# Kernel tuning notes

Hardware: AMD Instinct MI355X
Metric: run time of the kernel (lower is better)

The kernel has to match this reference:

```python
import jax, jax.numpy as jnp
import numpy as np


def _conv1x1(x, w, b):
    # x: (b, c_in, t, h, w); w: (c_out, c_in); b: (c_out,)
    return jnp.einsum('bcthw,oc->bothw', x, w) + b[None, :, None, None, None]


def _maxpool_hw(x):
    # MaxPool3d(kernel=(1,2,2)): pool spatial dims by 2 (h, w assumed even)
    b, c, t, h, w = x.shape
    return x.reshape(b, c, t, h // 2, 2, w // 2, 2).max(axis=(4, 6))


def setup_inputs() -> dict:
    key = jax.random.key(0)
    ks = jax.random.split(key, 9)
    C, CI = 256, 128  # in_channels, inter_channels = in_channels // 2
    B, T, H, W = 8, 8, 28, 28
    s = 1.0 / np.sqrt(C)
    si = 1.0 / np.sqrt(CI)
    return {
        'x': jax.random.normal(ks[0], (B, C, T, H, W), jnp.float32),
        'g_w': jax.random.normal(ks[1], (CI, C), jnp.float32) * s,
        'g_b': jax.random.normal(ks[2], (CI,), jnp.float32) * 0.01,
        'theta_w': jax.random.normal(ks[3], (CI, C), jnp.float32) * s,
        'theta_b': jax.random.normal(ks[4], (CI,), jnp.float32) * 0.01,
        'phi_w': jax.random.normal(ks[5], (CI, C), jnp.float32) * s,
        'phi_b': jax.random.normal(ks[6], (CI,), jnp.float32) * 0.01,
        'W_w': jax.random.normal(ks[7], (C, CI), jnp.float32) * si,
        'W_b': jax.random.normal(ks[8], (C,), jnp.float32) * 0.01,
    }


def reference(x, g_w, g_b, theta_w, theta_b, phi_w, phi_b, W_w, W_b):
    b, c, t, h, w = x.shape
    ci = g_w.shape[0]
    # g and phi paths are sub-sampled by MaxPool3d(1,2,2)
    g_x = _maxpool_hw(_conv1x1(x, g_w, g_b)).reshape(b, ci, -1)          # (b, ci, M)
    g_x = g_x.transpose(0, 2, 1)                                          # (b, M, ci)
    theta_x = _conv1x1(x, theta_w, theta_b).reshape(b, ci, -1)            # (b, ci, N)
    theta_x = theta_x.transpose(0, 2, 1)                                  # (b, N, ci)
    phi_x = _maxpool_hw(_conv1x1(x, phi_w, phi_b)).reshape(b, ci, -1)     # (b, ci, M)
    f = jnp.einsum('bnc,bcm->bnm', theta_x, phi_x)                        # (b, N, M)
    f_div_C = jax.nn.softmax(f, axis=-1)
    y = jnp.einsum('bnm,bmc->bnc', f_div_C, g_x)                          # (b, N, ci)
    y = y.transpose(0, 2, 1).reshape(b, ci, t, h, w)
    W_y = _conv1x1(y, W_w, W_b)
    return W_y + x
```

## Files before the change

### kernel.cpp

```cpp
#include <hip/hip_runtime.h>

typedef _Float16 f16;
typedef f16 half8 __attribute__((ext_vector_type(8)));
typedef __fp16 fp16x2 __attribute__((ext_vector_type(2)));
typedef float f32x4 __attribute__((ext_vector_type(4)));
typedef float f32x16 __attribute__((ext_vector_type(16)));

#define MFMA16(a, b, c) __builtin_amdgcn_mfma_f32_16x16x32_f16((a), (b), (c), 0, 0, 0)
#define MFMA32(a, b, c) __builtin_amdgcn_mfma_f32_32x32x16_f16((a), (b), (c), 0, 0, 0)

static constexpr int B = 8, C = 256, CI = 128, N = 6272, M = 1568, MP = 1600;

static constexpr size_t oXT = 0;
static constexpr size_t oQ  = (size_t)B * N * C;
static constexpr size_t oPF = oQ  + (size_t)B * N * CI;
static constexpr size_t oGF = oPF + (size_t)B * N * CI;
static constexpr size_t oPP = oGF + (size_t)B * N * CI;
static constexpr size_t oGT = oPP + (size_t)B * MP * CI;
static constexpr size_t oW  = oGT + (size_t)B * MP * CI;

static __device__ __forceinline__ half8 hmax8(half8 a, half8 b) {
    half8 r;
#pragma unroll
    for (int j = 0; j < 8; j++) r[j] = a[j] > b[j] ? a[j] : b[j];
    return r;
}

static __device__ __forceinline__ int pk2(float a, float b) {
    union { fp16x2 h; int i; } u;
    u.h = __builtin_amdgcn_cvt_pkrtz(a, b);
    return u.i;
}

__global__ void k_prep(const float* tw, const float* pw, const float* gw,
                       const float* Ww, f16* dst) {
    int i = blockIdx.x * 256 + threadIdx.x;
    int s = i >> 15, j = i & 32767;
    float v;
    if (s == 0) v = tw[j];
    else if (s == 1) v = pw[j];
    else if (s == 2) v = gw[j];
    else v = Ww[j];
    dst[i] = (f16)v;
}

__global__ __launch_bounds__(256, 2) void k_proj3(const float* __restrict__ x,
                                                  const f16* __restrict__ w16,
                                                  const float* __restrict__ tb,
                                                  const float* __restrict__ pb,
                                                  const float* __restrict__ gb,
                                                  f16* __restrict__ outQ,
                                                  f16* __restrict__ outP,
                                                  f16* __restrict__ outG) {
    __shared__ f16 xs[64 * 72];
    __shared__ f16 ws[3 * 128 * 72];
    int b = blockIdx.x, n0 = blockIdx.y * 64;
    int tid = threadIdx.x, w = tid >> 6, lane = tid & 63, ln = lane & 15, quad = lane >> 4;
    f32x4 acc[3][8];
#pragma unroll
    for (int p = 0; p < 3; p++)
#pragma unroll
        for (int cb = 0; cb < 8; cb++) acc[p][cb] = (f32x4){0.f, 0.f, 0.f, 0.f};

    for (int kc = 0; kc < 4; kc++) {
#pragma unroll
        for (int i = 0; i < 16; i++) {
            int qq = tid + i * 256;
            int nn = qq & 63, cc = qq >> 6;
            float v = x[(size_t)(b * C + kc * 64 + cc) * N + n0 + nn];
            xs[nn * 72 + cc] = (f16)v;
        }
#pragma unroll
        for (int p = 0; p < 3; p++)
#pragma unroll
            for (int i = 0; i < 4; i++) {
                int qq = tid + i * 256;
                int row = qq >> 3, coff = (qq & 7) * 8;
                *(int4*)&ws[p * 9216 + row * 72 + coff] =
                    *(const int4*)&w16[(size_t)p * 32768 + (size_t)row * C + kc * 64 + coff];
            }
        __syncthreads();
#pragma unroll
        for (int ks = 0; ks < 2; ks++) {
            half8 a = *(const half8*)&xs[(w * 16 + ln) * 72 + ks * 32 + quad * 8];
#pragma unroll
            for (int p = 0; p < 3; p++)
#pragma unroll
                for (int cb = 0; cb < 8; cb++) {
                    half8 bf = *(const half8*)&ws[p * 9216 + (cb * 16 + ln) * 72 + ks * 32 + quad * 8];
                    acc[p][cb] = MFMA16(a, bf, acc[p][cb]);
                }
        }
        __syncthreads();
    }
#pragma unroll
    for (int p = 0; p < 3; p++) {
        const float* bias = (p == 0) ? tb : (p == 1) ? pb : gb;
        f16* out = (p == 0) ? outQ : (p == 1) ? outP : outG;
#pragma unroll
        for (int cb = 0; cb < 8; cb++) {
            float bv = bias[cb * 16 + ln];
#pragma unroll
            for (int r = 0; r < 4; r++) {
                int n = n0 + w * 16 + quad * 4 + r;
                out[(size_t)(b * N + n) * CI + cb * 16 + ln] = (f16)(acc[p][cb][r] + bv);
            }
        }
    }
}

__global__ __launch_bounds__(256) void k_pool(const f16* __restrict__ phiF, const f16* __restrict__ gF,
                                              f16* __restrict__ phiP, f16* __restrict__ gPT) {
    __shared__ f16 gt[128 * 72];
    int b = blockIdx.x, mt = blockIdx.y;
    int tid = threadIdx.x;
#pragma unroll
    for (int i = 0; i < 4; i++) {
        int qq = tid + i * 256;
        int ml = qq >> 4, coff = (qq & 15) * 8;
        int m = mt * 64 + ml;
        half8 pv, gv;
        if (m < M) {
            int t = m / 196, rr = m % 196, hp = rr / 14, wp = rr % 14;
            int nb = t * 784 + hp * 56 + wp * 2;
            size_t base = ((size_t)(b * N) + nb) * CI + coff;
            half8 p0 = *(const half8*)&phiF[base];
            half8 p1 = *(const half8*)&phiF[base + CI];
            half8 p2 = *(const half8*)&phiF[base + 28 * CI];
            half8 p3 = *(const half8*)&phiF[base + 29 * CI];
            pv = hmax8(hmax8(p0, p1), hmax8(p2, p3));
            half8 g0 = *(const half8*)&gF[base];
            half8 g1 = *(const half8*)&gF[base + CI];
            half8 g2 = *(const half8*)&gF[base + 28 * CI];
            half8 g3 = *(const half8*)&gF[base + 29 * CI];
            gv = hmax8(hmax8(g0, g1), hmax8(g2, g3));
        } else {
#pragma unroll
            for (int j = 0; j < 8; j++) { pv[j] = (f16)0.f; gv[j] = (f16)0.f; }
        }
        *(half8*)&phiP[((size_t)b * MP + m) * CI + coff] = pv;
#pragma unroll
        for (int j = 0; j < 8; j++) gt[(coff + j) * 72 + ml] = gv[j];
    }
    __syncthreads();
#pragma unroll
    for (int i = 0; i < 4; i++) {
        int qq = tid + i * 256;
        int ci = qq >> 3, moff = (qq & 7) * 8;
        *(int4*)&gPT[((size_t)(b * CI) + ci) * MP + mt * 64 + moff] = *(const int4*)&gt[ci * 72 + moff];
    }
}

__global__ __launch_bounds__(256, 2) void k_attn(const f16* __restrict__ q,
                                                 const f16* __restrict__ kk,
                                                 const f16* __restrict__ v,
                                                 f16* __restrict__ y) {
    __shared__ f16 Ks[64 * 128];
    __shared__ f16 Vs[128 * 72];
    int b = blockIdx.x, n0 = blockIdx.y * 128;
    int tid = threadIdx.x, w = tid >> 6, lane = tid & 63;
    int l31 = lane & 31, hi = lane >> 5;
    int wq = n0 + w * 32;

    half8 qf[8];
#pragma unroll
    for (int kc = 0; kc < 8; kc++) {
        qf[kc] = *(const half8*)&q[(size_t)(b * N + wq + l31) * CI + kc * 16 + hi * 8];
#pragma unroll
        for (int j = 0; j < 8; j++) qf[kc][j] *= (f16)1.4426950408889634f;
    }

    f32x16 O0, O1, O2, O3;
#pragma unroll
    for (int i = 0; i < 16; i++) { O0[i] = 0.f; O1[i] = 0.f; O2[i] = 0.f; O3[i] = 0.f; }
    float Osum = 0.f, mi = -1e30f;

    for (int mc = 0; mc < 25; mc++) {
#pragma unroll
        for (int i = 0; i < 4; i++) {
            int qq = tid + i * 256;
            int kr = qq >> 4, c16 = qq & 15;
            *(int4*)&Ks[kr * 128 + ((c16 ^ (kr & 15)) << 3)] =
                *(const int4*)&kk[((size_t)b * MP + mc * 64 + kr) * CI + c16 * 8];
            int vr = qq >> 3, vc = (qq & 7) * 8;
            *(int4*)&Vs[vr * 72 + vc] = *(const int4*)&v[((size_t)(b * CI) + vr) * MP + mc * 64 + vc];
        }
        __syncthreads();

        f32x16 S0, S1;
#pragma unroll
        for (int i = 0; i < 16; i++) { S0[i] = 0.f; S1[i] = 0.f; }
        __builtin_amdgcn_s_setprio(1);
#pragma unroll
        for (int kc = 0; kc < 8; kc++) {
            int c16 = kc * 2 + hi;
            half8 a0 = *(const half8*)&Ks[l31 * 128 + ((c16 ^ (l31 & 15)) << 3)];
            half8 a1 = *(const half8*)&Ks[(32 + l31) * 128 + ((c16 ^ ((32 + l31) & 15)) << 3)];
            S0 = MFMA32(a0, qf[kc], S0);
            S1 = MFMA32(a1, qf[kc], S1);
        }
        __builtin_amdgcn_s_setprio(0);

        float vm = fmaxf(S0[0], S1[0]);
#pragma unroll
        for (int i = 1; i < 16; i++) vm = fmaxf(vm, fmaxf(S0[i], S1[i]));
        vm = fmaxf(vm, __shfl_xor(vm, 32));
        if (__ballot(vm > mi + 8.f)) {
            float mnew = fmaxf(mi, vm);
            float alpha = __builtin_amdgcn_exp2f(mi - mnew);
            mi = mnew;
            Osum *= alpha;
#pragma unroll
            for (int r = 0; r < 16; r++) {
                int qr = (r & 3) + 8 * (r >> 2) + 4 * hi;
                float al = __shfl(alpha, qr);
                O0[r] *= al; O1[r] *= al; O2[r] *= al; O3[r] *= al;
            }
        }
#pragma unroll
        for (int i = 0; i < 16; i++) {
            S0[i] = __builtin_amdgcn_exp2f(S0[i] - mi);
            S1[i] = __builtin_amdgcn_exp2f(S1[i] - mi);
        }
        if (mc == 24) {
#pragma unroll
            for (int i = 0; i < 16; i++) S1[i] = 0.f;
        }
        float ts = 0.f;
#pragma unroll
        for (int i = 0; i < 16; i++) ts += S0[i] + S1[i];
        ts += __shfl_xor(ts, 32);
        Osum += ts;

        __builtin_amdgcn_s_setprio(1);
#define PV_CHUNK(SV, RB, KC)                                                              \
        {                                                                                 \
            int a0 = pk2(SV[RB + 0], SV[RB + 1]);                                         \
            int a1 = pk2(SV[RB + 2], SV[RB + 3]);                                         \
            int a2 = pk2(SV[RB + 4], SV[RB + 5]);                                         \
            int a3 = pk2(SV[RB + 6], SV[RB + 7]);                                         \
            int b0 = __shfl_xor(a0, 32), b1 = __shfl_xor(a1, 32);                         \
            int b2 = __shfl_xor(a2, 32), b3 = __shfl_xor(a3, 32);                         \
            union { int4 i4; half8 h8; } u;                                               \
            u.i4.x = hi ? b2 : a0; u.i4.y = hi ? b3 : a1;                                 \
            u.i4.z = hi ? a2 : b0; u.i4.w = hi ? a3 : b1;                                 \
            O0 = MFMA32(u.h8, *(const half8*)&Vs[(0 * 32 + l31) * 72 + KC * 16 + hi * 8], O0); \
            O1 = MFMA32(u.h8, *(const half8*)&Vs[(1 * 32 + l31) * 72 + KC * 16 + hi * 8], O1); \
            O2 = MFMA32(u.h8, *(const half8*)&Vs[(2 * 32 + l31) * 72 + KC * 16 + hi * 8], O2); \
            O3 = MFMA32(u.h8, *(const half8*)&Vs[(3 * 32 + l31) * 72 + KC * 16 + hi * 8], O3); \
        }
        PV_CHUNK(S0, 0, 0)
        PV_CHUNK(S0, 8, 1)
        PV_CHUNK(S1, 0, 2)
        PV_CHUNK(S1, 8, 3)
#undef PV_CHUNK
        __builtin_amdgcn_s_setprio(0);
        __syncthreads();
    }

#pragma unroll
    for (int r = 0; r < 16; r++) {
        int qr = (r & 3) + 8 * (r >> 2) + 4 * hi;
        float inv = 1.0f / __shfl(Osum, qr);
        size_t base = (size_t)(b * N + wq + qr) * CI + l31;
        y[base]      = (f16)(O0[r] * inv);
        y[base + 32] = (f16)(O1[r] * inv);
        y[base + 64] = (f16)(O2[r] * inv);
        y[base + 96] = (f16)(O3[r] * inv);
    }
}

__global__ __launch_bounds__(256) void k_final(const f16* __restrict__ y,
                                               const f16* __restrict__ Ww,
                                               const float* __restrict__ Wb,
                                               const float* __restrict__ x,
                                               float* __restrict__ out) {
    __shared__ f16 ys[64 * 136];
    __shared__ f16 Ws[128 * 136];
    int b = blockIdx.x, ch = blockIdx.z, n0 = blockIdx.y * 64;
    int tid = threadIdx.x, w = tid >> 6, lane = tid & 63, ln = lane & 15, quad = lane >> 4;
#pragma unroll
    for (int i = 0; i < 4; i++) {
        int qq = tid + i * 256; int row = qq >> 4, coff = (qq & 15) * 8;
        *(int4*)&ys[row * 136 + coff] =
            *(const int4*)&y[(size_t)(b * N + n0 + row) * CI + coff];
    }
#pragma unroll
    for (int i = 0; i < 8; i++) {
        int qq = tid + i * 256; int row = qq >> 4, coff = (qq & 15) * 8;
        *(int4*)&Ws[row * 136 + coff] =
            *(const int4*)&Ww[(size_t)(ch * 128 + row) * CI + coff];
    }
    __syncthreads();
    f32x4 acc[2][4];
#pragma unroll
    for (int rb = 0; rb < 2; rb++)
#pragma unroll
        for (int nb = 0; nb < 4; nb++) acc[rb][nb] = (f32x4){0.f, 0.f, 0.f, 0.f};
#pragma unroll
    for (int ks = 0; ks < 4; ks++) {
        half8 a0 = *(const half8*)&Ws[(w * 32 + ln) * 136 + ks * 32 + quad * 8];
        half8 a1 = *(const half8*)&Ws[(w * 32 + 16 + ln) * 136 + ks * 32 + quad * 8];
#pragma unroll
        for (int nb = 0; nb < 4; nb++) {
            half8 bf = *(const half8*)&ys[(nb * 16 + ln) * 136 + ks * 32 + quad * 8];
            acc[0][nb] = MFMA16(a0, bf, acc[0][nb]);
            acc[1][nb] = MFMA16(a1, bf, acc[1][nb]);
        }
    }
#pragma unroll
    for (int rb = 0; rb < 2; rb++) {
        int cbase = ch * 128 + w * 32 + rb * 16 + quad * 4;
#pragma unroll
        for (int nb = 0; nb < 4; nb++) {
#pragma unroll
            for (int r = 0; r < 4; r++) {
                int c = cbase + r;
                size_t addr = (size_t)(b * C + c) * N + n0 + nb * 16 + ln;
                out[addr] = acc[rb][nb][r] + Wb[c] + x[addr];
            }
        }
    }
}

extern "C" void kernel_launch(void* const* d_in, const int* in_sizes, int n_in,
                              void* d_out, int out_size, void* d_ws, size_t ws_size,
                              hipStream_t stream) {
    const float* x  = (const float*)d_in[0];
    const float* gw = (const float*)d_in[1];
    const float* gb = (const float*)d_in[2];
    const float* tw = (const float*)d_in[3];
    const float* tb = (const float*)d_in[4];
    const float* pw = (const float*)d_in[5];
    const float* pb = (const float*)d_in[6];
    const float* Ww = (const float*)d_in[7];
    const float* Wb = (const float*)d_in[8];
    float* out = (float*)d_out;
    f16* ws = (f16*)d_ws;

    f16* Q    = ws + oQ;
    f16* phiF = ws + oPF;
    f16* gF   = ws + oGF;
    f16* phiP = ws + oPP;
    f16* gPT  = ws + oGT;
    f16* Y    = ws + oPF;
    f16* w16  = ws + oW;

    k_prep<<<512, 256, 0, stream>>>(tw, pw, gw, Ww, w16);
    k_proj3<<<dim3(8, 98), 256, 0, stream>>>(x, w16, tb, pb, gb, Q, phiF, gF);
    k_pool<<<dim3(8, 25), 256, 0, stream>>>(phiF, gF, phiP, gPT);
    k_attn<<<dim3(8, 49), 256, 0, stream>>>(Q, phiP, gPT, Y);
    k_final<<<dim3(8, 98, 2), 256, 0, stream>>>(Y, w16 + 98304, Wb, x, out);
    (void)in_sizes; (void)n_in; (void)out_size; (void)ws_size;
}
```

Baseline: 229.4 us.

## Double-buffer attention K/V tiles with direct global-to-LDS async loads

The attention kernel now keeps two LDS buffers for K and V and prefetches the next tile with global_load_lds while the current tile is computed, so load latency overlaps with the MFMA work. The V tile changes from a padded stride-72 layout to a 64-wide XOR-swizzled layout so the direct loads can write it without bank conflicts. LDS use per block roughly doubles, which may limit occupancy at 2 blocks per CU, and every iteration ends with a full vmcnt wait.

```diff
diff --git a/kernel.cpp b/kernel.cpp
--- a/kernel.cpp
+++ b/kernel.cpp
@@ -155,13 +155,35 @@
                                                  const f16* __restrict__ kk,
                                                  const f16* __restrict__ v,
                                                  f16* __restrict__ y) {
-    __shared__ f16 Ks[64 * 128];
-    __shared__ f16 Vs[128 * 72];
+    __shared__ f16 Ks[2][64 * 128];
+    __shared__ f16 Vs[2][128 * 64];
     int b = blockIdx.x, n0 = blockIdx.y * 128;
     int tid = threadIdx.x, w = tid >> 6, lane = tid & 63;
     int l31 = lane & 31, hi = lane >> 5;
     int wq = n0 + w * 32;
 
+#define STAGE(BUF, MC)                                                                     \
+    {                                                                                      \
+        _Pragma("unroll")                                                                  \
+        for (int i = 0; i < 4; i++) {                                                      \
+            int kr = w * 16 + i * 4 + (lane >> 4);                                         \
+            const f16* kg = kk + ((size_t)b * MP + (MC) * 64 + kr) * CI                    \
+                            + (((lane & 15) ^ (kr & 15)) << 3);                            \
+            __builtin_amdgcn_global_load_lds(                                              \
+                (const __attribute__((address_space(1))) void*)kg,                         \
+                (__attribute__((address_space(3))) void*)&Ks[BUF][w * 2048 + i * 512],     \
+                16, 0, 0);                                                                 \
+            int vr = w * 32 + i * 8 + (lane >> 3);                                         \
+            const f16* vg = v + ((size_t)(b * CI) + vr) * MP + (MC) * 64                   \
+                            + (((lane & 7) ^ (vr & 7)) << 3);                              \
+            __builtin_amdgcn_global_load_lds(                                              \
+                (const __attribute__((address_space(1))) void*)vg,                         \
+                (__attribute__((address_space(3))) void*)&Vs[BUF][w * 2048 + i * 512],     \
+                16, 0, 0);                                                                 \
+        }                                                                                  \
+    }
+
+    STAGE(0, 0)
     half8 qf[8];
 #pragma unroll
     for (int kc = 0; kc < 8; kc++) {
@@ -175,17 +197,12 @@
     for (int i = 0; i < 16; i++) { O0[i] = 0.f; O1[i] = 0.f; O2[i] = 0.f; O3[i] = 0.f; }
     float Osum = 0.f, mi = -1e30f;
 
+    asm volatile("s_waitcnt vmcnt(0)" ::: "memory");
+    __syncthreads();
+
+    int buf = 0;
     for (int mc = 0; mc < 25; mc++) {
-#pragma unroll
-        for (int i = 0; i < 4; i++) {
-            int qq = tid + i * 256;
-            int kr = qq >> 4, c16 = qq & 15;
-            *(int4*)&Ks[kr * 128 + ((c16 ^ (kr & 15)) << 3)] =
-                *(const int4*)&kk[((size_t)b * MP + mc * 64 + kr) * CI + c16 * 8];
-            int vr = qq >> 3, vc = (qq & 7) * 8;
-            *(int4*)&Vs[vr * 72 + vc] = *(const int4*)&v[((size_t)(b * CI) + vr) * MP + mc * 64 + vc];
-        }
-        __syncthreads();
+        if (mc < 24) STAGE(buf ^ 1, mc + 1)
 
         f32x16 S0, S1;
 #pragma unroll
@@ -194,8 +211,8 @@
 #pragma unroll
         for (int kc = 0; kc < 8; kc++) {
             int c16 = kc * 2 + hi;
-            half8 a0 = *(const half8*)&Ks[l31 * 128 + ((c16 ^ (l31 & 15)) << 3)];
-            half8 a1 = *(const half8*)&Ks[(32 + l31) * 128 + ((c16 ^ ((32 + l31) & 15)) << 3)];
+            half8 a0 = *(const half8*)&Ks[buf][l31 * 128 + ((c16 ^ (l31 & 15)) << 3)];
+            half8 a1 = *(const half8*)&Ks[buf][(32 + l31) * 128 + ((c16 ^ (l31 & 15)) << 3)];
             S0 = MFMA32(a0, qf[kc], S0);
             S1 = MFMA32(a1, qf[kc], S1);
         }
@@ -233,21 +250,21 @@
         Osum += ts;
 
         __builtin_amdgcn_s_setprio(1);
-#define PV_CHUNK(SV, RB, KC)                                                              \
-        {                                                                                 \
-            int a0 = pk2(SV[RB + 0], SV[RB + 1]);                                         \
-            int a1 = pk2(SV[RB + 2], SV[RB + 3]);                                         \
-            int a2 = pk2(SV[RB + 4], SV[RB + 5]);                                         \
-            int a3 = pk2(SV[RB + 6], SV[RB + 7]);                                         \
-            int b0 = __shfl_xor(a0, 32), b1 = __shfl_xor(a1, 32);                         \
-            int b2 = __shfl_xor(a2, 32), b3 = __shfl_xor(a3, 32);                         \
-            union { int4 i4; half8 h8; } u;                                               \
-            u.i4.x = hi ? b2 : a0; u.i4.y = hi ? b3 : a1;                                 \
-            u.i4.z = hi ? a2 : b0; u.i4.w = hi ? a3 : b1;                                 \
-            O0 = MFMA32(u.h8, *(const half8*)&Vs[(0 * 32 + l31) * 72 + KC * 16 + hi * 8], O0); \
-            O1 = MFMA32(u.h8, *(const half8*)&Vs[(1 * 32 + l31) * 72 + KC * 16 + hi * 8], O1); \
-            O2 = MFMA32(u.h8, *(const half8*)&Vs[(2 * 32 + l31) * 72 + KC * 16 + hi * 8], O2); \
-            O3 = MFMA32(u.h8, *(const half8*)&Vs[(3 * 32 + l31) * 72 + KC * 16 + hi * 8], O3); \
+#define PV_CHUNK(SV, RB, KC)                                                                   \
+        {                                                                                      \
+            int a0 = pk2(SV[RB + 0], SV[RB + 1]);                                              \
+            int a1 = pk2(SV[RB + 2], SV[RB + 3]);                                              \
+            int a2 = pk2(SV[RB + 4], SV[RB + 5]);                                              \
+            int a3 = pk2(SV[RB + 6], SV[RB + 7]);                                              \
+            int b0 = __shfl_xor(a0, 32), b1 = __shfl_xor(a1, 32);                              \
+            int b2 = __shfl_xor(a2, 32), b3 = __shfl_xor(a3, 32);                              \
+            union { int4 i4; half8 h8; } u;                                                    \
+            u.i4.x = hi ? b2 : a0; u.i4.y = hi ? b3 : a1;                                      \
+            u.i4.z = hi ? a2 : b0; u.i4.w = hi ? a3 : b1;                                      \
+            O0 = MFMA32(u.h8, *(const half8*)&Vs[buf][(0 * 32 + l31) * 64 + ((((KC) * 2 + hi) ^ (l31 & 7)) << 3)], O0); \
+            O1 = MFMA32(u.h8, *(const half8*)&Vs[buf][(1 * 32 + l31) * 64 + ((((KC) * 2 + hi) ^ (l31 & 7)) << 3)], O1); \
+            O2 = MFMA32(u.h8, *(const half8*)&Vs[buf][(2 * 32 + l31) * 64 + ((((KC) * 2 + hi) ^ (l31 & 7)) << 3)], O2); \
+            O3 = MFMA32(u.h8, *(const half8*)&Vs[buf][(3 * 32 + l31) * 64 + ((((KC) * 2 + hi) ^ (l31 & 7)) << 3)], O3); \
         }
         PV_CHUNK(S0, 0, 0)
         PV_CHUNK(S0, 8, 1)
@@ -255,8 +272,12 @@
         PV_CHUNK(S1, 8, 3)
 #undef PV_CHUNK
         __builtin_amdgcn_s_setprio(0);
+
+        asm volatile("s_waitcnt vmcnt(0)" ::: "memory");
         __syncthreads();
-    }
+        buf ^= 1;
+    }
+#undef STAGE
 
 #pragma unroll
     for (int r = 0; r < 16; r++) {
```

Measured after the change: 228.5 us. No clear change (-0.4%).

## Split attention key tiles across two wave groups and merge softmax partials

Applied to the files above, without the earlier changes.

The attention kernel goes from 256 to 512 threads per block. Two groups of four waves each take half of every 64-key tile, and each group keeps its own online-softmax state. At the end, group 1 writes its normalized output, max and sum to shared memory, and group 0 merges them with rescaling before storing. This doubles the waves available to hide latency on only 392 blocks, at the cost of a final merge, a larger register footprint per CU, and duplicated Q fragments.

```diff
diff --git a/kernel.cpp b/kernel.cpp
--- a/kernel.cpp
+++ b/kernel.cpp
@@ -151,16 +151,19 @@
     }
 }
 
-__global__ __launch_bounds__(256, 2) void k_attn(const f16* __restrict__ q,
+__global__ __launch_bounds__(512, 4) void k_attn(const f16* __restrict__ q,
                                                  const f16* __restrict__ kk,
                                                  const f16* __restrict__ v,
                                                  f16* __restrict__ y) {
-    __shared__ f16 Ks[64 * 128];
-    __shared__ f16 Vs[128 * 72];
+    __shared__ f16 smem[17408];
+    f16* Ks = smem;
+    f16* Vs = smem + 8192;
     int b = blockIdx.x, n0 = blockIdx.y * 128;
     int tid = threadIdx.x, w = tid >> 6, lane = tid & 63;
     int l31 = lane & 31, hi = lane >> 5;
-    int wq = n0 + w * 32;
+    int grp = w >> 2, wl = w & 3;
+    int wq = n0 + wl * 32;
+    int mrow = grp * 32 + l31;
 
     half8 qf[8];
 #pragma unroll
@@ -177,8 +180,8 @@
 
     for (int mc = 0; mc < 25; mc++) {
 #pragma unroll
-        for (int i = 0; i < 4; i++) {
-            int qq = tid + i * 256;
+        for (int i = 0; i < 2; i++) {
+            int qq = tid + i * 512;
             int kr = qq >> 4, c16 = qq & 15;
             *(int4*)&Ks[kr * 128 + ((c16 ^ (kr & 15)) << 3)] =
                 *(const int4*)&kk[((size_t)b * MP + mc * 64 + kr) * CI + c16 * 8];
@@ -187,23 +190,21 @@
         }
         __syncthreads();
 
-        f32x16 S0, S1;
-#pragma unroll
-        for (int i = 0; i < 16; i++) { S0[i] = 0.f; S1[i] = 0.f; }
+        f32x16 S;
+#pragma unroll
+        for (int i = 0; i < 16; i++) S[i] = 0.f;
         __builtin_amdgcn_s_setprio(1);
 #pragma unroll
         for (int kc = 0; kc < 8; kc++) {
             int c16 = kc * 2 + hi;
-            half8 a0 = *(const half8*)&Ks[l31 * 128 + ((c16 ^ (l31 & 15)) << 3)];
-            half8 a1 = *(const half8*)&Ks[(32 + l31) * 128 + ((c16 ^ ((32 + l31) & 15)) << 3)];
-            S0 = MFMA32(a0, qf[kc], S0);
-            S1 = MFMA32(a1, qf[kc], S1);
+            half8 a = *(const half8*)&Ks[mrow * 128 + ((c16 ^ (mrow & 15)) << 3)];
+            S = MFMA32(a, qf[kc], S);
         }
         __builtin_amdgcn_s_setprio(0);
 
-        float vm = fmaxf(S0[0], S1[0]);
-#pragma unroll
-        for (int i = 1; i < 16; i++) vm = fmaxf(vm, fmaxf(S0[i], S1[i]));
+        float vm = S[0];
+#pragma unroll
+        for (int i = 1; i < 16; i++) vm = fmaxf(vm, S[i]);
         vm = fmaxf(vm, __shfl_xor(vm, 32));
         if (__ballot(vm > mi + 8.f)) {
             float mnew = fmaxf(mi, vm);
@@ -218,55 +219,77 @@
             }
         }
 #pragma unroll
-        for (int i = 0; i < 16; i++) {
-            S0[i] = __builtin_amdgcn_exp2f(S0[i] - mi);
-            S1[i] = __builtin_amdgcn_exp2f(S1[i] - mi);
-        }
-        if (mc == 24) {
-#pragma unroll
-            for (int i = 0; i < 16; i++) S1[i] = 0.f;
+        for (int i = 0; i < 16; i++) S[i] = __builtin_amdgcn_exp2f(S[i] - mi);
+        if (mc == 24 && grp) {
+#pragma unroll
+            for (int i = 0; i < 16; i++) S[i] = 0.f;
         }
         float ts = 0.f;
 #pragma unroll
-        for (int i = 0; i < 16; i++) ts += S0[i] + S1[i];
+        for (int i = 0; i < 16; i++) ts += S[i];
         ts += __shfl_xor(ts, 32);
         Osum += ts;
 
         __builtin_amdgcn_s_setprio(1);
-#define PV_CHUNK(SV, RB, KC)                                                              \
-        {                                                                                 \
-            int a0 = pk2(SV[RB + 0], SV[RB + 1]);                                         \
-            int a1 = pk2(SV[RB + 2], SV[RB + 3]);                                         \
-            int a2 = pk2(SV[RB + 4], SV[RB + 5]);                                         \
-            int a3 = pk2(SV[RB + 6], SV[RB + 7]);                                         \
-            int b0 = __shfl_xor(a0, 32), b1 = __shfl_xor(a1, 32);                         \
-            int b2 = __shfl_xor(a2, 32), b3 = __shfl_xor(a3, 32);                         \
-            union { int4 i4; half8 h8; } u;                                               \
-            u.i4.x = hi ? b2 : a0; u.i4.y = hi ? b3 : a1;                                 \
-            u.i4.z = hi ? a2 : b0; u.i4.w = hi ? a3 : b1;                                 \
-            O0 = MFMA32(u.h8, *(const half8*)&Vs[(0 * 32 + l31) * 72 + KC * 16 + hi * 8], O0); \
-            O1 = MFMA32(u.h8, *(const half8*)&Vs[(1 * 32 + l31) * 72 + KC * 16 + hi * 8], O1); \
-            O2 = MFMA32(u.h8, *(const half8*)&Vs[(2 * 32 + l31) * 72 + KC * 16 + hi * 8], O2); \
-            O3 = MFMA32(u.h8, *(const half8*)&Vs[(3 * 32 + l31) * 72 + KC * 16 + hi * 8], O3); \
-        }
-        PV_CHUNK(S0, 0, 0)
-        PV_CHUNK(S0, 8, 1)
-        PV_CHUNK(S1, 0, 2)
-        PV_CHUNK(S1, 8, 3)
+#define PV_CHUNK(SV, RB, KC)                                                                   \
+        {                                                                                      \
+            int a0 = pk2(SV[RB + 0], SV[RB + 1]);                                              \
+            int a1 = pk2(SV[RB + 2], SV[RB + 3]);                                              \
+            int a2 = pk2(SV[RB + 4], SV[RB + 5]);                                              \
+            int a3 = pk2(SV[RB + 6], SV[RB + 7]);                                              \
+            int b0 = __shfl_xor(a0, 32), b1 = __shfl_xor(a1, 32);                              \
+            int b2 = __shfl_xor(a2, 32), b3 = __shfl_xor(a3, 32);                              \
+            union { int4 i4; half8 h8; } u;                                                    \
+            u.i4.x = hi ? b2 : a0; u.i4.y = hi ? b3 : a1;                                      \
+            u.i4.z = hi ? a2 : b0; u.i4.w = hi ? a3 : b1;                                      \
+            O0 = MFMA32(u.h8, *(const half8*)&Vs[(0 * 32 + l31) * 72 + (KC) * 16 + hi * 8], O0); \
+            O1 = MFMA32(u.h8, *(const half8*)&Vs[(1 * 32 + l31) * 72 + (KC) * 16 + hi * 8], O1); \
+            O2 = MFMA32(u.h8, *(const half8*)&Vs[(2 * 32 + l31) * 72 + (KC) * 16 + hi * 8], O2); \
+            O3 = MFMA32(u.h8, *(const half8*)&Vs[(3 * 32 + l31) * 72 + (KC) * 16 + hi * 8], O3); \
+        }
+        PV_CHUNK(S, 0, 2 * grp)
+        PV_CHUNK(S, 8, 2 * grp + 1)
 #undef PV_CHUNK
         __builtin_amdgcn_s_setprio(0);
         __syncthreads();
     }
 
-#pragma unroll
-    for (int r = 0; r < 16; r++) {
-        int qr = (r & 3) + 8 * (r >> 2) + 4 * hi;
-        float inv = 1.0f / __shfl(Osum, qr);
-        size_t base = (size_t)(b * N + wq + qr) * CI + l31;
-        y[base]      = (f16)(O0[r] * inv);
-        y[base + 32] = (f16)(O1[r] * inv);
-        y[base + 64] = (f16)(O2[r] * inv);
-        y[base + 96] = (f16)(O3[r] * inv);
+    f16* OB = smem;
+    float* mB = (float*)(smem + 16384);
+    float* sB = mB + 128;
+    if (grp == 1) {
+#pragma unroll
+        for (int r = 0; r < 16; r++) {
+            int qr = (r & 3) + 8 * (r >> 2) + 4 * hi;
+            float is = 1.0f / __shfl(Osum, qr);
+            int qloc = wl * 32 + qr;
+            OB[qloc * 128 + l31]      = (f16)(O0[r] * is);
+            OB[qloc * 128 + 32 + l31] = (f16)(O1[r] * is);
+            OB[qloc * 128 + 64 + l31] = (f16)(O2[r] * is);
+            OB[qloc * 128 + 96 + l31] = (f16)(O3[r] * is);
+        }
+        mB[wl * 32 + l31] = mi;
+        sB[wl * 32 + l31] = Osum;
+    }
+    __syncthreads();
+    if (grp == 0) {
+#pragma unroll
+        for (int r = 0; r < 16; r++) {
+            int qr = (r & 3) + 8 * (r >> 2) + 4 * hi;
+            int qloc = wl * 32 + qr;
+            float mA = __shfl(mi, qr), sA = __shfl(Osum, qr);
+            float mBq = mB[qloc], sBq = sB[qloc];
+            float m = fmaxf(mA, mBq);
+            float al = __builtin_amdgcn_exp2f(mA - m);
+            float be = __builtin_amdgcn_exp2f(mBq - m);
+            float denom = sA * al + sBq * be;
+            float cA = al / denom, cB = sBq * be / denom;
+            size_t base = (size_t)(b * N + wq + qr) * CI + l31;
+            y[base]      = (f16)(O0[r] * cA + (float)OB[qloc * 128 + l31] * cB);
+            y[base + 32] = (f16)(O1[r] * cA + (float)OB[qloc * 128 + 32 + l31] * cB);
+            y[base + 64] = (f16)(O2[r] * cA + (float)OB[qloc * 128 + 64 + l31] * cB);
+            y[base + 96] = (f16)(O3[r] * cA + (float)OB[qloc * 128 + 96 + l31] * cB);
+        }
     }
 }
 
@@ -349,7 +372,7 @@
     k_prep<<<512, 256, 0, stream>>>(tw, pw, gw, Ww, w16);
     k_proj3<<<dim3(8, 98), 256, 0, stream>>>(x, w16, tb, pb, gb, Q, phiF, gF);
     k_pool<<<dim3(8, 25), 256, 0, stream>>>(phiF, gF, phiP, gPT);
-    k_attn<<<dim3(8, 49), 256, 0, stream>>>(Q, phiP, gPT, Y);
+    k_attn<<<dim3(8, 49), 512, 0, stream>>>(Q, phiP, gPT, Y);
     k_final<<<dim3(8, 98, 2), 256, 0, stream>>>(Y, w16 + 98304, Wb, x, out);
     (void)in_sizes; (void)n_in; (void)out_size; (void)ws_size;
 }
```

Result: slower. 327.7 us (+42.8%).
